# Kernel optimization log

Hardware: AMD Instinct MI355X
Metric: run time of the kernel (lower is better)

Reference implementation:

```python
import jax, jax.numpy as jnp
import numpy as np

# dims
B, V, IMG = 16, 2, 224
G, PATCH, SG = 7, 14, 16
D, NH, L = 768, 12, 12
DH = D // NH            # 64
P = DH // 4             # rope frequencies per axis (2D axial RoPE)
N = G * G               # 49 glimpse tokens
S = SG * SG             # 256 scene tokens
GSIZE = G * PATCH       # 98 px glimpse


def _ln(x, w, b):
    m = x.mean(-1, keepdims=True)
    v = ((x - m) ** 2).mean(-1, keepdims=True)
    return (x - m) * jax.lax.rsqrt(v + 1e-6) * w + b


def _rope(pos, periods):
    # pos [B,N,2] -> cos,sin [B,N,2P]  (x freqs then y freqs)
    ang = (pos[..., :, None] / periods).reshape(pos.shape[0], pos.shape[1], -1)
    return jnp.cos(ang), jnp.sin(ang)


def _apply_rope(x, cos, sin):
    # x [B,H,N,DH]; cos/sin [B,N,DH//2]
    c = cos[:, None, :, :]
    s = sin[:, None, :, :]
    xr = x.reshape(x.shape[0], x.shape[1], x.shape[2], DH // 2, 2)
    x1, x2 = xr[..., 0], xr[..., 1]
    return jnp.stack([x1 * c - x2 * s, x1 * s + x2 * c], -1).reshape(x.shape)


def _heads(x):
    return x.reshape(x.shape[0], x.shape[1], NH, DH).transpose(0, 2, 1, 3)


def _merge(x):
    return x.transpose(0, 2, 1, 3).reshape(x.shape[0], x.shape[2], D)


def _attn(q, k, v):
    a = jax.nn.softmax(jnp.einsum('bhqd,bhkd->bhqk', q, k) / jnp.sqrt(jnp.float32(DH)), axis=-1)
    return jnp.einsum('bhqk,bhkd->bhqd', a, v)


def _cross(xq, xkv, qw, qb, kvw, kvb, ow, ob, rq, rkv):
    q = _heads(xq @ qw.T + qb)
    kv = xkv @ kvw.T + kvb
    k, v = _heads(kv[..., :D]), _heads(kv[..., D:])
    q = _apply_rope(q, *rq)
    k = _apply_rope(k, *rkv)
    return _merge(_attn(q, k, v)) @ ow.T + ob


def _bilinear(img, py, px):
    # img [C,H,W], py/px [GSIZE] pixel coords -> [C,GSIZE,GSIZE]
    Hh, Ww = img.shape[1], img.shape[2]
    y0 = jnp.clip(jnp.floor(py), 0, Hh - 2).astype(jnp.int32)
    x0 = jnp.clip(jnp.floor(px), 0, Ww - 2).astype(jnp.int32)
    wy = jnp.clip(py - y0, 0.0, 1.0)[None, :, None]
    wx = jnp.clip(px - x0, 0.0, 1.0)[None, None, :]
    g0, g1 = img[:, y0, :], img[:, y0 + 1, :]
    v00, v01 = g0[:, :, x0], g0[:, :, x0 + 1]
    v10, v11 = g1[:, :, x0], g1[:, :, x0 + 1]
    return (v00 * (1 - wy) + v10 * wy) * (1 - wx) + (v01 * (1 - wy) + v11 * wy) * wx


def _extract(images, c, s):
    # crop a [-1,1]-normalized glimpse of half-width `scale` at `center`
    lin = jnp.linspace(-1.0, 1.0, GSIZE)
    gy = c[:, 1:2] + s[:, None] * lin
    gx = c[:, 0:1] + s[:, None] * lin
    py = (gy + 1.0) * 0.5 * (images.shape[2] - 1)
    px = (gx + 1.0) * 0.5 * (images.shape[3] - 1)
    return jax.vmap(_bilinear)(images, py, px)


def _forward(images, centers, scales, patch_w, patch_b, scene_tokens,
             ln1_w, ln1_b, ln2_w, ln2_b, qkv_w, qkv_b, attn_out_w, attn_out_b,
             mlp_w1, mlp_b1, mlp_w2, mlp_b2,
             read_q_w, read_q_b, read_kv_w, read_kv_b, read_out_w, read_out_b, read_gate,
             write_q_w, write_q_b, write_kv_w, write_kv_b, write_out_w, write_out_b, write_gate):
    periods = 100.0 ** (jnp.arange(P, dtype=jnp.float32) / P)
    lin_s = jnp.linspace(-1.0, 1.0, SG)
    ys, xs = jnp.meshgrid(lin_s, lin_s, indexing='ij')
    scene_pos = jnp.broadcast_to(jnp.stack([xs.ravel(), ys.ravel()], -1), (B, S, 2))
    scene_rope = _rope(scene_pos, periods)
    lin_g = jnp.linspace(-1.0, 1.0, G)
    yg, xg = jnp.meshgrid(lin_g, lin_g, indexing='ij')
    goffs = jnp.stack([xg.ravel(), yg.ravel()], -1)  # [N,2]

    scene = jnp.broadcast_to(scene_tokens, (B, S, D))
    for vp in range(V):
        glimpse = _extract(images, centers[vp], scales[vp])  # [B,3,98,98]
        t = jax.lax.conv_general_dilated(glimpse, patch_w, (PATCH, PATCH), 'VALID',
                                         dimension_numbers=('NCHW', 'OIHW', 'NCHW'))
        local = t.reshape(B, D, N).transpose(0, 2, 1) + patch_b  # [B,49,D]
        lpos = centers[vp][:, None, :] + scales[vp][:, None, None] * goffs
        lrope = _rope(lpos, periods)
        for i in range(L):
            local = local + read_gate[i] * _cross(local, scene,
                read_q_w[i], read_q_b[i], read_kv_w[i], read_kv_b[i],
                read_out_w[i], read_out_b[i], lrope, scene_rope)
            # ViT block with RoPE self-attention
            h = _ln(local, ln1_w[i], ln1_b[i])
            qkv = h @ qkv_w[i].T + qkv_b[i]
            q, k, v = _heads(qkv[..., :D]), _heads(qkv[..., D:2 * D]), _heads(qkv[..., 2 * D:])
            q = _apply_rope(q, *lrope)
            k = _apply_rope(k, *lrope)
            local = local + _merge(_attn(q, k, v)) @ attn_out_w[i].T + attn_out_b[i]
            h = _ln(local, ln2_w[i], ln2_b[i])
            local = local + jax.nn.gelu(h @ mlp_w1[i].T + mlp_b1[i]) @ mlp_w2[i].T + mlp_b2[i]
            scene = scene + write_gate[i] * _cross(scene, local,
                write_q_w[i], write_q_b[i], write_kv_w[i], write_kv_b[i],
                write_out_w[i], write_out_b[i], scene_rope, lrope)
    return scene  # [B,S,D]


def setup_inputs() -> dict:
    key = jax.random.key(0)
    ks = iter(jax.random.split(key, 40))
    std = 0.02
    d = {}
    d['images'] = jax.random.normal(next(ks), (B, 3, IMG, IMG), jnp.float32)
    d['centers'] = jax.random.uniform(next(ks), (V, B, 2), jnp.float32, -0.5, 0.5)
    d['scales'] = jax.random.uniform(next(ks), (V, B), jnp.float32, 0.2, 0.4)
    d['patch_w'] = jax.random.normal(next(ks), (D, 3, PATCH, PATCH), jnp.float32) * std
    d['patch_b'] = jnp.zeros((D,), jnp.float32)
    d['scene_tokens'] = jax.random.normal(next(ks), (1, S, D), jnp.float32) / jnp.sqrt(jnp.float32(D))
    d['ln1_w'] = jnp.ones((L, D), jnp.float32); d['ln1_b'] = jnp.zeros((L, D), jnp.float32)
    d['ln2_w'] = jnp.ones((L, D), jnp.float32); d['ln2_b'] = jnp.zeros((L, D), jnp.float32)
    d['qkv_w'] = jax.random.normal(next(ks), (L, 3 * D, D), jnp.float32) * std
    d['qkv_b'] = jnp.zeros((L, 3 * D), jnp.float32)
    d['attn_out_w'] = jax.random.normal(next(ks), (L, D, D), jnp.float32) * std
    d['attn_out_b'] = jnp.zeros((L, D), jnp.float32)
    d['mlp_w1'] = jax.random.normal(next(ks), (L, 4 * D, D), jnp.float32) * std
    d['mlp_b1'] = jnp.zeros((L, 4 * D), jnp.float32)
    d['mlp_w2'] = jax.random.normal(next(ks), (L, D, 4 * D), jnp.float32) * std
    d['mlp_b2'] = jnp.zeros((L, D), jnp.float32)
    for pre in ('read', 'write'):
        d[pre + '_q_w'] = jax.random.normal(next(ks), (L, D, D), jnp.float32) * std
        d[pre + '_q_b'] = jnp.zeros((L, D), jnp.float32)
        d[pre + '_kv_w'] = jax.random.normal(next(ks), (L, 2 * D, D), jnp.float32) * std
        d[pre + '_kv_b'] = jnp.zeros((L, 2 * D), jnp.float32)
        d[pre + '_out_w'] = jax.random.normal(next(ks), (L, D, D), jnp.float32) * std
        d[pre + '_out_b'] = jnp.zeros((L, D), jnp.float32)
        d[pre + '_gate'] = jax.random.normal(next(ks), (L, D), jnp.float32) * 0.1
    return d


def reference(images, centers, scales, patch_w, patch_b, scene_tokens,
              ln1_w, ln1_b, ln2_w, ln2_b, qkv_w, qkv_b, attn_out_w, attn_out_b,
              mlp_w1, mlp_b1, mlp_w2, mlp_b2,
              read_q_w, read_q_b, read_kv_w, read_kv_b, read_out_w, read_out_b, read_gate,
              write_q_w, write_q_b, write_kv_w, write_kv_b, write_out_w, write_out_b, write_gate):
    return _forward(images, centers, scales, patch_w, patch_b, scene_tokens,
                    ln1_w, ln1_b, ln2_w, ln2_b, qkv_w, qkv_b, attn_out_w, attn_out_b,
                    mlp_w1, mlp_b1, mlp_w2, mlp_b2,
                    read_q_w, read_q_b, read_kv_w, read_kv_b, read_out_w, read_out_b, read_gate,
                    write_q_w, write_q_b, write_kv_w, write_kv_b, write_out_w, write_out_b, write_gate)
```

## Files before the change

kernel.cpp:

```cpp
#include <hip/hip_runtime.h>

#define B_ 16
#define V_ 2
#define D_ 768
#define NH_ 12
#define L_ 12
#define DH_ 64
#define N_ 49
#define S_ 256

__device__ __forceinline__ unsigned short f2bf(float f) {
  unsigned int u = __builtin_bit_cast(unsigned int, f);
  u += 0x7fffu + ((u >> 16) & 1u);
  return (unsigned short)(u >> 16);
}
__device__ __forceinline__ float bf2f(unsigned short h) {
  unsigned int u = ((unsigned int)h) << 16;
  return __builtin_bit_cast(float, u);
}
__device__ __forceinline__ float bflo(unsigned int w) {
  return __builtin_bit_cast(float, w << 16);
}
__device__ __forceinline__ float bfhi(unsigned int w) {
  return __builtin_bit_cast(float, w & 0xffff0000u);
}
__device__ __forceinline__ unsigned int packbf2(float a, float b) {
  return (unsigned int)f2bf(a) | ((unsigned int)f2bf(b) << 16);
}

using bf16x8 = __attribute__((ext_vector_type(8))) __bf16;
using u16x8  = __attribute__((ext_vector_type(8))) unsigned short;
using f32x4  = __attribute__((ext_vector_type(4))) float;

__device__ __forceinline__ void g2l16(const unsigned short* g, unsigned short* l) {
  __builtin_amdgcn_global_load_lds(
      (const __attribute__((address_space(1))) unsigned int*)g,
      (__attribute__((address_space(3))) unsigned int*)l, 16, 0, 0);
}

template <int BM, int BN, int BK>
__global__ __launch_bounds__(256) void gemm_v4(
    const unsigned short* __restrict__ A, int lda,
    const unsigned short* __restrict__ W, int ldw,
    const float* __restrict__ bias,
    float* __restrict__ Cf, unsigned short* __restrict__ Cb, int ldc,
    const float* __restrict__ res, const float* __restrict__ gate,
    int M, int N, int K, int epi)
{
  __shared__ unsigned short As[2][BM * BK];
  __shared__ unsigned short Bs[2][BN * BK];
  constexpr int FM = BM / 32, FN = BN / 32;
  constexpr int CPR = BK / 8;
  constexpr int LPS = (BM + BN) * BK / 2048;
  const int m0 = blockIdx.x * BM, n0 = blockIdx.y * BN;
  const int tid = threadIdx.x, lane = tid & 63, wid = tid >> 6;
  const int wr = wid >> 1, wc = wid & 1;
  const int fr = lane & 15, kq8 = lane >> 4;

  f32x4 acc[FM][FN];
#pragma unroll
  for (int mi = 0; mi < FM; ++mi)
#pragma unroll
    for (int ni = 0; ni < FN; ++ni) acc[mi][ni] = f32x4{0.f, 0.f, 0.f, 0.f};

  auto stage = [&](int buf, int k0) {
    const unsigned short* Ab = A + (size_t)m0 * lda + k0;
    const unsigned short* Bb = W + (size_t)n0 * ldw + k0;
#pragma unroll
    for (int ra = 0; ra < BM * BK / 2048; ++ra) {
      int c = ra * 256 + tid;
      int row = c / CPR, slot = c % CPR;
      int gslot = slot ^ (row & 7);
      g2l16(Ab + (size_t)row * lda + gslot * 8, &As[buf][c * 8]);
    }
#pragma unroll
    for (int rb = 0; rb < BN * BK / 2048; ++rb) {
      int c = rb * 256 + tid;
      int row = c / CPR, slot = c % CPR;
      int gslot = slot ^ (row & 7);
      g2l16(Bb + (size_t)row * ldw + gslot * 8, &Bs[buf][c * 8]);
    }
  };

  const int nt = K / BK;
  stage(0, 0);
  int cur = 0;
  for (int t = 0; t < nt; ++t) {
    if (t + 1 < nt) {
      stage(cur ^ 1, (t + 1) * BK);
      asm volatile("s_waitcnt vmcnt(%0)" :: "i"(LPS) : "memory");
    } else {
      asm volatile("s_waitcnt vmcnt(0)" ::: "memory");
    }
    __builtin_amdgcn_s_barrier();
#pragma unroll
    for (int ks = 0; ks < BK / 32; ++ks) {
      bf16x8 av[FM], bv[FN];
#pragma unroll
      for (int mi = 0; mi < FM; ++mi) {
        int row = wr * (BM / 2) + mi * 16 + fr;
        int idx = row * BK + (((ks * 4 + kq8) ^ (row & 7)) << 3);
        av[mi] = __builtin_bit_cast(bf16x8, *(const u16x8*)&As[cur][idx]);
      }
#pragma unroll
      for (int ni = 0; ni < FN; ++ni) {
        int row = wc * (BN / 2) + ni * 16 + fr;
        int idx = row * BK + (((ks * 4 + kq8) ^ (row & 7)) << 3);
        bv[ni] = __builtin_bit_cast(bf16x8, *(const u16x8*)&Bs[cur][idx]);
      }
#pragma unroll
      for (int mi = 0; mi < FM; ++mi)
#pragma unroll
        for (int ni = 0; ni < FN; ++ni)
          acc[mi][ni] = __builtin_amdgcn_mfma_f32_16x16x32_bf16(av[mi], bv[ni], acc[mi][ni], 0, 0, 0);
    }
    __builtin_amdgcn_s_barrier();
    cur ^= 1;
  }

  const int er = (lane >> 4) * 4, ec = lane & 15;
#pragma unroll
  for (int mi = 0; mi < FM; ++mi)
#pragma unroll
    for (int ni = 0; ni < FN; ++ni) {
      int gc = n0 + wc * (BN / 2) + ni * 16 + ec;
      float bi = bias ? bias[gc] : 0.0f;
      float gg = gate ? gate[gc] : 1.0f;
#pragma unroll
      for (int i = 0; i < 4; ++i) {
        int gr = m0 + wr * (BM / 2) + mi * 16 + er + i;
        if (gr < M) {
          float v = acc[mi][ni][i] + bi;
          if (epi == 1) {
            v = v / (1.0f + __expf(-1.59576912f * (v + 0.044715f * v * v * v)));
          } else if (epi == 2) {
            v = res[(size_t)gr * ldc + gc] + gg * v;
          }
          if (Cf) Cf[(size_t)gr * ldc + gc] = v;
          if (Cb) Cb[(size_t)gr * ldc + gc] = f2bf(v);
        }
      }
    }
}

template <int LKPAD>
__global__ __launch_bounds__(256) void attn_mfma(
    const unsigned short* __restrict__ Q, int ldq, int qoff, int Lq,
    const unsigned short* __restrict__ KV, int ldkv, int koff, int voff, int Lk,
    const float* __restrict__ cq, const float* __restrict__ sq, int rbq,
    const float* __restrict__ ck, const float* __restrict__ sk, int rbk,
    unsigned short* __restrict__ Out)
{
  constexpr int NT = LKPAD / 16;
  constexpr int NKS = LKPAD / 32;
  __shared__ unsigned short Kb[LKPAD * 64];
  __shared__ unsigned short Vt[64 * LKPAD];
  __shared__ unsigned short Qs[4][16 * 64];
  __shared__ unsigned short Pl[4][16 * LKPAD];
  const int b = blockIdx.x / NH_, h = blockIdx.x - b * NH_;
  const int tid = threadIdx.x, lane = tid & 63, wid = tid >> 6;

  for (int idx = tid; idx < LKPAD * 32; idx += 256) {
    int t = idx >> 5, m = idx & 31;
    int d = 2 * m;
    int ksl = (t << 6) + (((m >> 2) ^ (t & 7)) << 3) + ((m & 3) << 1);
    int vs0 = d * LKPAD + (((t >> 3) ^ (d & 7)) << 3) + (t & 7);
    int vs1 = (d + 1) * LKPAD + (((t >> 3) ^ ((d + 1) & 7)) << 3) + (t & 7);
    if (t < Lk) {
      size_t rowb = ((size_t)b * Lk + t) * ldkv;
      unsigned int kw = *(const unsigned int*)(KV + rowb + koff + h * DH_ + d);
      unsigned int vw = *(const unsigned int*)(KV + rowb + voff + h * DH_ + d);
      float k1 = bflo(kw), k2 = bfhi(kw);
      size_t ri = (size_t)b * rbk + (size_t)t * 32 + m;
      float c = ck[ri], s = sk[ri];
      *(unsigned int*)&Kb[ksl] = packbf2((k1 * c - k2 * s) * 0.125f, (k1 * s + k2 * c) * 0.125f);
      Vt[vs0] = (unsigned short)(vw & 0xffff);
      Vt[vs1] = (unsigned short)(vw >> 16);
    } else {
      *(unsigned int*)&Kb[ksl] = 0;
      Vt[vs0] = 0; Vt[vs1] = 0;
    }
  }
  const int qbase = blockIdx.y * 64 + wid * 16;
  for (int idx = lane; idx < 16 * 32; idx += 64) {
    int r = idx >> 5, m = idx & 31;
    int gq = qbase + r;
    unsigned int qr = 0;
    if (gq < Lq) {
      unsigned int qw = *(const unsigned int*)(Q + ((size_t)b * Lq + gq) * ldq + qoff + h * DH_ + 2 * m);
      float q1 = bflo(qw), q2 = bfhi(qw);
      size_t ri = (size_t)b * rbq + (size_t)gq * 32 + m;
      float c = cq[ri], s = sq[ri];
      qr = packbf2(q1 * c - q2 * s, q1 * s + q2 * c);
    }
    *(unsigned int*)&Qs[wid][(r << 6) + (((m >> 2) ^ (r & 7)) << 3) + ((m & 3) << 1)] = qr;
  }
  __syncthreads();

  const int fr = lane & 15, g = lane >> 4;
  bf16x8 qa[2];
#pragma unroll
  for (int ks = 0; ks < 2; ++ks)
    qa[ks] = __builtin_bit_cast(bf16x8,
        *(const u16x8*)&Qs[wid][(fr << 6) + ((((ks << 2) + g) ^ (fr & 7)) << 3)]);

  f32x4 sv[NT];
  __builtin_amdgcn_s_setprio(1);
#pragma unroll
  for (int t = 0; t < NT; ++t) {
    int key = (t << 4) + fr;
    f32x4 a = {0.f, 0.f, 0.f, 0.f};
#pragma unroll
    for (int ks = 0; ks < 2; ++ks) {
      bf16x8 kb = __builtin_bit_cast(bf16x8,
          *(const u16x8*)&Kb[(key << 6) + ((((ks << 2) + g) ^ (key & 7)) << 3)]);
      a = __builtin_amdgcn_mfma_f32_16x16x32_bf16(qa[ks], kb, a, 0, 0, 0);
    }
    sv[t] = a;
  }
  __builtin_amdgcn_s_setprio(0);
#pragma unroll
  for (int t = 0; t < NT; ++t) {
    int key = (t << 4) + fr;
    if (key >= Lk) sv[t] = f32x4{-1e30f, -1e30f, -1e30f, -1e30f};
  }
  f32x4 mx = sv[0];
#pragma unroll
  for (int t = 1; t < NT; ++t)
#pragma unroll
    for (int i = 0; i < 4; ++i) mx[i] = fmaxf(mx[i], sv[t][i]);
#pragma unroll
  for (int off = 1; off <= 8; off <<= 1)
#pragma unroll
    for (int i = 0; i < 4; ++i) mx[i] = fmaxf(mx[i], __shfl_xor(mx[i], off));
  f32x4 sm = {0.f, 0.f, 0.f, 0.f};
#pragma unroll
  for (int t = 0; t < NT; ++t)
#pragma unroll
    for (int i = 0; i < 4; ++i) {
      float e = __expf(sv[t][i] - mx[i]);
      sv[t][i] = e;
      sm[i] += e;
    }
#pragma unroll
  for (int off = 1; off <= 8; off <<= 1)
#pragma unroll
    for (int i = 0; i < 4; ++i) sm[i] += __shfl_xor(sm[i], off);
  f32x4 inv;
#pragma unroll
  for (int i = 0; i < 4; ++i) inv[i] = 1.0f / sm[i];
#pragma unroll
  for (int t = 0; t < NT; ++t) {
    int key = (t << 4) + fr;
    int chunk = key >> 3;
#pragma unroll
    for (int i = 0; i < 4; ++i) {
      int row = (g << 2) + i;
      Pl[wid][row * LKPAD + ((chunk ^ (row & 7)) << 3) + (key & 7)] = f2bf(sv[t][i]);
    }
  }
  f32x4 oacc[4];
#pragma unroll
  for (int n = 0; n < 4; ++n) oacc[n] = f32x4{0.f, 0.f, 0.f, 0.f};
  __builtin_amdgcn_s_setprio(1);
#pragma unroll
  for (int ks = 0; ks < NKS; ++ks) {
    int chunk = (ks << 2) + g;
    bf16x8 pa = __builtin_bit_cast(bf16x8,
        *(const u16x8*)&Pl[wid][fr * LKPAD + ((chunk ^ (fr & 7)) << 3)]);
#pragma unroll
    for (int n = 0; n < 4; ++n) {
      int drow = (n << 4) + fr;
      bf16x8 vb = __builtin_bit_cast(bf16x8,
          *(const u16x8*)&Vt[drow * LKPAD + ((chunk ^ (drow & 7)) << 3)]);
      oacc[n] = __builtin_amdgcn_mfma_f32_16x16x32_bf16(pa, vb, oacc[n], 0, 0, 0);
    }
  }
  __builtin_amdgcn_s_setprio(0);
#pragma unroll
  for (int n = 0; n < 4; ++n)
#pragma unroll
    for (int i = 0; i < 4; ++i) {
      int gq = qbase + (g << 2) + i;
      if (gq < Lq)
        Out[((size_t)b * Lq + gq) * D_ + h * DH_ + (n << 4) + fr] = f2bf(oacc[n][i] * inv[i]);
    }
}

__global__ __launch_bounds__(256) void ln_kernel(
    const float* __restrict__ X, const float* __restrict__ w,
    const float* __restrict__ bsh, unsigned short* __restrict__ Out)
{
  const int row = blockIdx.x, tid = threadIdx.x;
  const float* x = X + (size_t)row * D_;
  float v0 = x[tid], v1 = x[tid + 256], v2 = x[tid + 512];
  __shared__ float red[4];
  float s = v0 + v1 + v2;
  for (int o = 32; o; o >>= 1) s += __shfl_xor(s, o);
  if ((tid & 63) == 0) red[tid >> 6] = s;
  __syncthreads();
  float mean = (red[0] + red[1] + red[2] + red[3]) * (1.0f / 768.0f);
  float d0 = v0 - mean, d1 = v1 - mean, d2 = v2 - mean;
  float q = d0 * d0 + d1 * d1 + d2 * d2;
  __syncthreads();
  for (int o = 32; o; o >>= 1) q += __shfl_xor(q, o);
  if ((tid & 63) == 0) red[tid >> 6] = q;
  __syncthreads();
  float var = (red[0] + red[1] + red[2] + red[3]) * (1.0f / 768.0f);
  float rstd = rsqrtf(var + 1e-6f);
  Out[(size_t)row * D_ + tid]       = f2bf(d0 * rstd * w[tid]       + bsh[tid]);
  Out[(size_t)row * D_ + tid + 256] = f2bf(d1 * rstd * w[tid + 256] + bsh[tid + 256]);
  Out[(size_t)row * D_ + tid + 512] = f2bf(d2 * rstd * w[tid + 512] + bsh[tid + 512]);
}

struct CvtA {
  const float* s[10];
  unsigned short* d[10];
  unsigned int lsrc[10];
  unsigned int lstride[10];
  int blkEnd[10];
};
__global__ __launch_bounds__(256) void cvt_multi_k(CvtA c) {
  int bid = blockIdx.x;
  int seg = 0;
#pragma unroll
  for (int i = 0; i < 9; ++i) seg += (bid >= c.blkEnd[i]) ? 1 : 0;
  unsigned int e = (unsigned int)(bid - (seg ? c.blkEnd[seg - 1] : 0)) * 2048u
                   + (unsigned int)threadIdx.x * 8u;
  unsigned int l = e / c.lsrc[seg], r = e - l * c.lsrc[seg];
  const float* s = c.s[seg] + e;
  unsigned short* d = c.d[seg] + (size_t)l * c.lstride[seg] + r;
  f32x4 a = *(const f32x4*)s, b2 = *(const f32x4*)(s + 4);
  u16x8 o;
  o[0] = f2bf(a.x); o[1] = f2bf(a.y); o[2] = f2bf(a.z); o[3] = f2bf(a.w);
  o[4] = f2bf(b2.x); o[5] = f2bf(b2.y); o[6] = f2bf(b2.z); o[7] = f2bf(b2.w);
  *(u16x8*)d = o;
}

__global__ void cvt_patch_k(const float* __restrict__ s, unsigned short* __restrict__ d) {
  int i = blockIdx.x * 256 + threadIdx.x;
  if (i >= 768 * 768) return;
  int r = i / 768, col = i - r * 768;
  d[i] = f2bf(col < 588 ? s[r * 588 + col] : 0.0f);
}

__global__ void fbias_k(const float* __restrict__ wqb, const float* __restrict__ rkvb,
                        float* __restrict__ fb) {
  int i = blockIdx.x * 256 + threadIdx.x;
  if (i >= L_ * 2304) return;
  int l = i / 2304, c = i - l * 2304;
  fb[i] = (c < 768) ? wqb[l * 768 + c] : rkvb[l * 1536 + (c - 768)];
}

__global__ void init_scene_k(const float* __restrict__ tok, float* __restrict__ sf,
                             unsigned short* __restrict__ sb, int total) {
  int i = blockIdx.x * 256 + threadIdx.x;
  if (i < total) {
    float v = tok[i % (S_ * D_)];
    sf[i] = v; sb[i] = f2bf(v);
  }
}

__global__ void rope_scene_k(float* __restrict__ c, float* __restrict__ s) {
  int idx = blockIdx.x * 256 + threadIdx.x;
  if (idx >= S_ * 32) return;
  int t = idx >> 5, m = idx & 31;
  int i = t >> 4, j = t & 15;
  float xx = -1.0f + 2.0f * j / 15.0f;
  float yy = -1.0f + 2.0f * i / 15.0f;
  float coord = (m < 16) ? xx : yy;
  float per = powf(100.0f, (float)(m & 15) / 16.0f);
  float ang = coord / per;
  c[idx] = cosf(ang); s[idx] = sinf(ang);
}

__global__ void rope_local_k(float* __restrict__ c, float* __restrict__ s,
                             const float* __restrict__ ctr, const float* __restrict__ scl) {
  int idx = blockIdx.x * 256 + threadIdx.x;
  if (idx >= B_ * N_ * 32) return;
  int b = idx / (N_ * 32);
  int r = idx - b * (N_ * 32);
  int pch = r >> 5, m = r & 31;
  int py = pch / 7, px = pch - py * 7;
  float cx = ctr[b * 2], cy = ctr[b * 2 + 1], sc = scl[b];
  float gx = cx + sc * ((px - 3.0f) / 3.0f);
  float gy = cy + sc * ((py - 3.0f) / 3.0f);
  float coord = (m < 16) ? gx : gy;
  float per = powf(100.0f, (float)(m & 15) / 16.0f);
  float ang = coord / per;
  c[idx] = cosf(ang); s[idx] = sinf(ang);
}

__global__ void im2col_k(unsigned short* __restrict__ xb, const float* __restrict__ img,
                         const float* __restrict__ ctr, const float* __restrict__ scl) {
  int idx = blockIdx.x * 256 + threadIdx.x;
  if (idx >= 784 * 768) return;
  int row = idx / 768, col = idx - row * 768;
  float val = 0.0f;
  if (col < 588) {
    int b = row / 49, pch = row - b * 49;
    int c = col / 196, rr = col - c * 196;
    int i = rr / 14, j = rr - i * 14;
    int py = pch / 7, px = pch - py * 7;
    int gyi = py * 14 + i, gxi = px * 14 + j;
    float cx = ctr[b * 2], cy = ctr[b * 2 + 1], sc = scl[b];
    float gy = cy + sc * (-1.0f + 2.0f * gyi / 97.0f);
    float gx = cx + sc * (-1.0f + 2.0f * gxi / 97.0f);
    float pyi = (gy + 1.0f) * 0.5f * 223.0f;
    float pxi = (gx + 1.0f) * 0.5f * 223.0f;
    float y0f = fminf(fmaxf(floorf(pyi), 0.0f), 222.0f);
    float x0f = fminf(fmaxf(floorf(pxi), 0.0f), 222.0f);
    int y0 = (int)y0f, x0 = (int)x0f;
    float wy = fminf(fmaxf(pyi - y0f, 0.0f), 1.0f);
    float wx = fminf(fmaxf(pxi - x0f, 0.0f), 1.0f);
    const float* base = img + (size_t)(b * 3 + c) * 224 * 224;
    float v00 = base[y0 * 224 + x0],       v01 = base[y0 * 224 + x0 + 1];
    float v10 = base[(y0 + 1) * 224 + x0], v11 = base[(y0 + 1) * 224 + x0 + 1];
    val = (v00 * (1.0f - wy) + v10 * wy) * (1.0f - wx) + (v01 * (1.0f - wy) + v11 * wy) * wx;
  }
  xb[idx] = f2bf(val);
}

extern "C" void kernel_launch(void* const* d_in, const int* in_sizes, int n_in,
                              void* d_out, int out_size, void* d_ws, size_t ws_size,
                              hipStream_t stream) {
  const float* images    = (const float*)d_in[0];
  const float* centers   = (const float*)d_in[1];
  const float* scales    = (const float*)d_in[2];
  const float* patch_w   = (const float*)d_in[3];
  const float* patch_b   = (const float*)d_in[4];
  const float* scene_tok = (const float*)d_in[5];
  const float* ln1_w = (const float*)d_in[6];
  const float* ln1_b = (const float*)d_in[7];
  const float* ln2_w = (const float*)d_in[8];
  const float* ln2_b = (const float*)d_in[9];
  const float* qkv_w = (const float*)d_in[10];
  const float* qkv_b = (const float*)d_in[11];
  const float* ao_w  = (const float*)d_in[12];
  const float* ao_b  = (const float*)d_in[13];
  const float* m1_w  = (const float*)d_in[14];
  const float* m1_b  = (const float*)d_in[15];
  const float* m2_w  = (const float*)d_in[16];
  const float* m2_b  = (const float*)d_in[17];
  const float* rq_w  = (const float*)d_in[18];
  const float* rq_b  = (const float*)d_in[19];
  const float* rkv_w = (const float*)d_in[20];
  const float* rkv_b = (const float*)d_in[21];
  const float* ro_w  = (const float*)d_in[22];
  const float* ro_b  = (const float*)d_in[23];
  const float* rgate = (const float*)d_in[24];
  const float* wq_w  = (const float*)d_in[25];
  const float* wq_b  = (const float*)d_in[26];
  const float* wkv_w = (const float*)d_in[27];
  const float* wkv_b = (const float*)d_in[28];
  const float* wo_w  = (const float*)d_in[29];
  const float* wo_b  = (const float*)d_in[30];
  const float* wgate = (const float*)d_in[31];

  float* scene_f = (float*)d_out;

  char* p = (char*)d_ws;
  auto alloc = [&](size_t bytes) { char* r = p; p += (bytes + 255) & ~(size_t)255; return (void*)r; };
  unsigned short* scene_bf = (unsigned short*)alloc((size_t)4096 * 768 * 2);
  float*          local_f  = (float*)alloc((size_t)784 * 768 * 4);
  unsigned short* local_bf = (unsigned short*)alloc((size_t)832 * 768 * 2);
  unsigned short* q_r_bf   = (unsigned short*)alloc((size_t)784 * 768 * 2);
  unsigned short* qrkv_bf  = (unsigned short*)alloc((size_t)4096 * 2304 * 2);
  unsigned short* kv_bf    = (unsigned short*)alloc((size_t)784 * 2304 * 2);
  unsigned short* ln_bf    = (unsigned short*)alloc((size_t)832 * 768 * 2);
  unsigned short* act_bf   = (unsigned short*)alloc((size_t)4096 * 768 * 2);
  unsigned short* x_bf     = (unsigned short*)alloc((size_t)832 * 768 * 2);
  float* sc_cos = (float*)alloc((size_t)S_ * 32 * 4);
  float* sc_sin = (float*)alloc((size_t)S_ * 32 * 4);
  float* l_cos  = (float*)alloc((size_t)B_ * N_ * 32 * 4);
  float* l_sin  = (float*)alloc((size_t)B_ * N_ * 32 * 4);
  unsigned short* patch_wbf = (unsigned short*)alloc((size_t)768 * 768 * 2);
  float*          fb        = (float*)alloc((size_t)L_ * 2304 * 4);

  static const unsigned int LSRC[10] = {589824, 589824, 1179648, 589824, 1769472,
                                        589824, 2359296, 2359296, 1179648, 589824};
  static const unsigned int LSTR[10] = {589824, 1769472, 1769472, 589824, 1769472,
                                        589824, 2359296, 2359296, 1179648, 589824};
  static const unsigned int DOFF[10] = {0, 0, 589824, 0, 0, 0, 0, 0, 0, 0};
  const float* WSRC[10] = {rq_w, wq_w, rkv_w, ro_w, qkv_w, ao_w, m1_w, m2_w, wkv_w, wo_w};
  static const size_t REGSZ[9] = {589824, 1769472, 589824, 1769472, 589824,
                                  2359296, 2359296, 1179648, 589824};
  size_t regBase[9];
  size_t allElemsPerLayer = 0;
  {
    size_t cur = 0;
    for (int i = 0; i < 9; ++i) { regBase[i] = cur; cur += REGSZ[i] * L_; allElemsPerLayer += REGSZ[i]; }
  }
  const size_t allElems = allElemsPerLayer * L_;
  size_t usedBytes = (size_t)(p - (char*)d_ws);
  bool preconv = ws_size >= usedBytes + allElems * 2 + 4096;
  unsigned short* wbf = (unsigned short*)alloc((preconv ? allElems : allElemsPerLayer) * 2);

  enum { T128, T128x64, T64 };
  auto G = [&](int tile, const unsigned short* A, int lda, const unsigned short* Wp, int ldw,
               const float* bias, float* Cf, unsigned short* Cb, int ldc,
               const float* res, const float* gt, int M, int N, int K, int epi) {
    if (tile == T128)
      gemm_v4<128, 128, 64><<<dim3(M / 128, N / 128), 256, 0, stream>>>(
          A, lda, Wp, ldw, bias, Cf, Cb, ldc, res, gt, M, N, K, epi);
    else if (tile == T128x64)
      gemm_v4<128, 64, 64><<<dim3(M / 128, N / 64), 256, 0, stream>>>(
          A, lda, Wp, ldw, bias, Cf, Cb, ldc, res, gt, M, N, K, epi);
    else
      gemm_v4<64, 64, 128><<<dim3((M + 63) / 64, N / 64), 256, 0, stream>>>(
          A, lda, Wp, ldw, bias, Cf, Cb, ldc, res, gt, M, N, K, epi);
  };

  {
    int total = B_ * S_ * D_;
    init_scene_k<<<(total + 255) / 256, 256, 0, stream>>>(scene_tok, scene_f, scene_bf, total);
    rope_scene_k<<<(S_ * 32 + 255) / 256, 256, 0, stream>>>(sc_cos, sc_sin);
    cvt_patch_k<<<(768 * 768 + 255) / 256, 256, 0, stream>>>(patch_w, patch_wbf);
    fbias_k<<<(L_ * 2304 + 255) / 256, 256, 0, stream>>>(wq_b, rkv_b, fb);
    if (preconv) {
      CvtA cv;
      int blk = 0;
      for (int i = 0; i < 10; ++i) {
        int reg = i >= 2 ? i - 1 : i;
        cv.s[i] = WSRC[i];
        cv.d[i] = wbf + regBase[reg] + DOFF[i];
        cv.lsrc[i] = LSRC[i];
        cv.lstride[i] = LSTR[i];
        blk += (int)((size_t)LSRC[i] * L_ / 2048);
        cv.blkEnd[i] = blk;
      }
      cvt_multi_k<<<blk, 256, 0, stream>>>(cv);
    }
  }

  for (int vp = 0; vp < V_; ++vp) {
    const float* ctr = centers + (size_t)vp * B_ * 2;
    const float* scl = scales + (size_t)vp * B_;
    rope_local_k<<<(B_ * N_ * 32 + 255) / 256, 256, 0, stream>>>(l_cos, l_sin, ctr, scl);
    im2col_k<<<(784 * 768 + 255) / 256, 256, 0, stream>>>(x_bf, images, ctr, scl);
    G(T64, x_bf, 768, patch_wbf, 768, patch_b, local_f, local_bf, 768,
      nullptr, nullptr, 784, 768, 768, 0);

    for (int l = 0; l < L_; ++l) {
      const unsigned short* wL[10];
      if (preconv) {
        for (int i = 0; i < 10; ++i) {
          int reg = i >= 2 ? i - 1 : i;
          wL[i] = wbf + regBase[reg] + (size_t)l * LSTR[i] + DOFF[i];
        }
      } else {
        CvtA cv;
        int blk = 0;
        size_t cur = 0;
        size_t rb[9];
        for (int i = 0; i < 10; ++i) {
          int reg = i >= 2 ? i - 1 : i;
          if (i != 2) { rb[reg] = cur; cur += REGSZ[reg]; }
          cv.s[i] = WSRC[i] + (size_t)l * LSRC[i];
          cv.d[i] = wbf + rb[reg] + DOFF[i];
          cv.lsrc[i] = LSRC[i];
          cv.lstride[i] = LSTR[i];
          blk += (int)(LSRC[i] / 2048);
          cv.blkEnd[i] = blk;
          wL[i] = (unsigned short*)cv.d[i];
        }
        cvt_multi_k<<<blk, 256, 0, stream>>>(cv);
      }
      const unsigned short *w_rq = wL[0], *w_qrkv = wL[1], *w_ro = wL[3], *w_qkv = wL[4],
                           *w_ao = wL[5], *w_m1 = wL[6], *w_m2 = wL[7], *w_wkv = wL[8],
                           *w_wo = wL[9];

      G(T128, scene_bf, 768, w_qrkv, 768, fb + (size_t)l * 2304,
        nullptr, qrkv_bf, 2304, nullptr, nullptr, 4096, 2304, 768, 0);
      G(T64, local_bf, 768, w_rq, 768, rq_b + l * 768,
        nullptr, q_r_bf, 768, nullptr, nullptr, 784, 768, 768, 0);
      attn_mfma<256><<<dim3(B_ * NH_, 1), 256, 0, stream>>>(q_r_bf, 768, 0, 49,
          qrkv_bf, 2304, 768, 1536, 256, l_cos, l_sin, N_ * 32, sc_cos, sc_sin, 0, act_bf);
      G(T64, act_bf, 768, w_ro, 768, ro_b + l * 768,
        local_f, local_bf, 768, local_f, rgate + l * 768, 784, 768, 768, 2);
      ln_kernel<<<784, 256, 0, stream>>>(local_f, ln1_w + l * 768, ln1_b + l * 768, ln_bf);
      G(T64, ln_bf, 768, w_qkv, 768, qkv_b + (size_t)l * 2304,
        nullptr, kv_bf, 2304, nullptr, nullptr, 784, 2304, 768, 0);
      attn_mfma<64><<<dim3(B_ * NH_, 1), 256, 0, stream>>>(kv_bf, 2304, 0, 49,
          kv_bf, 2304, 768, 1536, 49, l_cos, l_sin, N_ * 32, l_cos, l_sin, N_ * 32, act_bf);
      G(T64, act_bf, 768, w_ao, 768, ao_b + l * 768,
        local_f, local_bf, 768, local_f, nullptr, 784, 768, 768, 2);
      ln_kernel<<<784, 256, 0, stream>>>(local_f, ln2_w + l * 768, ln2_b + l * 768, ln_bf);
      G(T64, ln_bf, 768, w_m1, 768, m1_b + (size_t)l * 3072,
        nullptr, act_bf, 3072, nullptr, nullptr, 784, 3072, 768, 1);
      G(T64, act_bf, 3072, w_m2, 3072, m2_b + l * 768,
        local_f, local_bf, 768, local_f, nullptr, 784, 768, 3072, 2);
      G(T64, local_bf, 768, w_wkv, 768, wkv_b + (size_t)l * 1536,
        nullptr, kv_bf, 1536, nullptr, nullptr, 784, 1536, 768, 0);
      attn_mfma<64><<<dim3(B_ * NH_, 4), 256, 0, stream>>>(qrkv_bf, 2304, 0, 256,
          kv_bf, 1536, 0, 768, 49, sc_cos, sc_sin, 0, l_cos, l_sin, N_ * 32, act_bf);
      G(T128x64, act_bf, 768, w_wo, 768, wo_b + l * 768,
        scene_f, scene_bf, 768, scene_f, wgate + l * 768, 4096, 768, 768, 2);
    }
  }
}
```

Before: 6.534 ms.

## Fuse next-layer read-Q into write-KV GEMM, swizzle GEMM workgroups across XCDs, retile

Adds an XCD-aware remapping of workgroup ids in the GEMM so neighbouring tiles land on the same chiplet, aiming for better L2 reuse. The next layer's read-query projection weights are concatenated onto the write-KV weights, so one GEMM yields both and the separate read-Q GEMM runs only at layer 0. GEMM tiles change to BK=128 with 128x128 for scene GEMMs and 128x64 for local ones. Local buffers are padded to 896 rows for the larger M tile. This adds bias and weight layout complexity and may reduce occupancy through the larger LDS tiles.

```diff
diff --git a/kernel.cpp b/kernel.cpp
--- a/kernel.cpp
+++ b/kernel.cpp
@@ -39,7 +39,7 @@
 }
 
 template <int BM, int BN, int BK>
-__global__ __launch_bounds__(256) void gemm_v4(
+__global__ __launch_bounds__(256) void gemm_v5(
     const unsigned short* __restrict__ A, int lda,
     const unsigned short* __restrict__ W, int ldw,
     const float* __restrict__ bias,
@@ -52,7 +52,14 @@
   constexpr int FM = BM / 32, FN = BN / 32;
   constexpr int CPR = BK / 8;
   constexpr int LPS = (BM + BN) * BK / 2048;
-  const int m0 = blockIdx.x * BM, n0 = blockIdx.y * BN;
+  const int gx = gridDim.x;
+  const int nwg = gx * gridDim.y;
+  const int orig = blockIdx.y * gx + blockIdx.x;
+  const int xcd = orig & 7, rem = orig >> 3;
+  const int qq = nwg >> 3, rr = nwg & 7;
+  const int wgid = (xcd < rr ? xcd * (qq + 1) : rr * (qq + 1) + (xcd - rr) * qq) + rem;
+  const int m0 = (wgid % gx) * BM, n0 = (wgid / gx) * BN;
+
   const int tid = threadIdx.x, lane = tid & 63, wid = tid >> 6;
   const int wr = wid >> 1, wc = wid & 1;
   const int fr = lane & 15, kq8 = lane >> 4;
@@ -314,17 +321,17 @@
 }
 
 struct CvtA {
-  const float* s[10];
-  unsigned short* d[10];
-  unsigned int lsrc[10];
-  unsigned int lstride[10];
-  int blkEnd[10];
+  const float* s[11];
+  unsigned short* d[11];
+  unsigned int lsrc[11];
+  unsigned int lstride[11];
+  int blkEnd[11];
 };
 __global__ __launch_bounds__(256) void cvt_multi_k(CvtA c) {
   int bid = blockIdx.x;
   int seg = 0;
 #pragma unroll
-  for (int i = 0; i < 9; ++i) seg += (bid >= c.blkEnd[i]) ? 1 : 0;
+  for (int i = 0; i < 10; ++i) seg += (bid >= c.blkEnd[i]) ? 1 : 0;
   unsigned int e = (unsigned int)(bid - (seg ? c.blkEnd[seg - 1] : 0)) * 2048u
                    + (unsigned int)threadIdx.x * 8u;
   unsigned int l = e / c.lsrc[seg], r = e - l * c.lsrc[seg];
@@ -350,6 +357,14 @@
   if (i >= L_ * 2304) return;
   int l = i / 2304, c = i - l * 2304;
   fb[i] = (c < 768) ? wqb[l * 768 + c] : rkvb[l * 1536 + (c - 768)];
+}
+
+__global__ void fbias2_k(const float* __restrict__ wkvb, const float* __restrict__ rqb,
+                         float* __restrict__ fb2) {
+  int i = blockIdx.x * 256 + threadIdx.x;
+  if (i >= L_ * 2304) return;
+  int l = i / 2304, c = i - l * 2304;
+  fb2[i] = (c < 1536) ? wkvb[l * 1536 + c] : rqb[((l + 1) % L_) * 768 + (c - 1536)];
 }
 
 __global__ void init_scene_k(const float* __restrict__ tok, float* __restrict__ sf,
@@ -463,52 +478,60 @@
   auto alloc = [&](size_t bytes) { char* r = p; p += (bytes + 255) & ~(size_t)255; return (void*)r; };
   unsigned short* scene_bf = (unsigned short*)alloc((size_t)4096 * 768 * 2);
   float*          local_f  = (float*)alloc((size_t)784 * 768 * 4);
-  unsigned short* local_bf = (unsigned short*)alloc((size_t)832 * 768 * 2);
-  unsigned short* q_r_bf   = (unsigned short*)alloc((size_t)784 * 768 * 2);
+  unsigned short* local_bf = (unsigned short*)alloc((size_t)896 * 768 * 2);
+  unsigned short* q_r_bf   = (unsigned short*)alloc((size_t)896 * 768 * 2);
   unsigned short* qrkv_bf  = (unsigned short*)alloc((size_t)4096 * 2304 * 2);
-  unsigned short* kv_bf    = (unsigned short*)alloc((size_t)784 * 2304 * 2);
-  unsigned short* ln_bf    = (unsigned short*)alloc((size_t)832 * 768 * 2);
+  unsigned short* kv_bf    = (unsigned short*)alloc((size_t)896 * 2304 * 2);
+  unsigned short* kvq_bf   = (unsigned short*)alloc((size_t)896 * 2304 * 2);
+  unsigned short* ln_bf    = (unsigned short*)alloc((size_t)896 * 768 * 2);
   unsigned short* act_bf   = (unsigned short*)alloc((size_t)4096 * 768 * 2);
-  unsigned short* x_bf     = (unsigned short*)alloc((size_t)832 * 768 * 2);
+  unsigned short* x_bf     = (unsigned short*)alloc((size_t)896 * 768 * 2);
   float* sc_cos = (float*)alloc((size_t)S_ * 32 * 4);
   float* sc_sin = (float*)alloc((size_t)S_ * 32 * 4);
   float* l_cos  = (float*)alloc((size_t)B_ * N_ * 32 * 4);
   float* l_sin  = (float*)alloc((size_t)B_ * N_ * 32 * 4);
   unsigned short* patch_wbf = (unsigned short*)alloc((size_t)768 * 768 * 2);
   float*          fb        = (float*)alloc((size_t)L_ * 2304 * 4);
-
-  static const unsigned int LSRC[10] = {589824, 589824, 1179648, 589824, 1769472,
-                                        589824, 2359296, 2359296, 1179648, 589824};
-  static const unsigned int LSTR[10] = {589824, 1769472, 1769472, 589824, 1769472,
-                                        589824, 2359296, 2359296, 1179648, 589824};
-  static const unsigned int DOFF[10] = {0, 0, 589824, 0, 0, 0, 0, 0, 0, 0};
-  const float* WSRC[10] = {rq_w, wq_w, rkv_w, ro_w, qkv_w, ao_w, m1_w, m2_w, wkv_w, wo_w};
+  float*          fb2       = (float*)alloc((size_t)L_ * 2304 * 4);
+
   static const size_t REGSZ[9] = {589824, 1769472, 589824, 1769472, 589824,
-                                  2359296, 2359296, 1179648, 589824};
+                                  2359296, 2359296, 1769472, 589824};
+  struct SegDef { const float* src; int reg; unsigned off; unsigned lsrc; int nl; };
+  const SegDef SEGS[11] = {
+    {rq_w,            0, 0,       589824,  L_},
+    {wq_w,            1, 0,       589824,  L_},
+    {rkv_w,           1, 589824,  1179648, L_},
+    {ro_w,            2, 0,       589824,  L_},
+    {qkv_w,           3, 0,       1769472, L_},
+    {ao_w,            4, 0,       589824,  L_},
+    {m1_w,            5, 0,       2359296, L_},
+    {m2_w,            6, 0,       2359296, L_},
+    {wkv_w,           7, 0,       1179648, L_},
+    {rq_w + 589824,   7, 1179648, 589824,  L_ - 1},
+    {wo_w,            8, 0,       589824,  L_},
+  };
   size_t regBase[9];
-  size_t allElemsPerLayer = 0;
+  size_t perLayer = 0;
   {
     size_t cur = 0;
-    for (int i = 0; i < 9; ++i) { regBase[i] = cur; cur += REGSZ[i] * L_; allElemsPerLayer += REGSZ[i]; }
-  }
-  const size_t allElems = allElemsPerLayer * L_;
+    for (int i = 0; i < 9; ++i) { regBase[i] = cur; cur += REGSZ[i] * L_; perLayer += REGSZ[i]; }
+  }
+  const size_t allElems = perLayer * L_;
   size_t usedBytes = (size_t)(p - (char*)d_ws);
   bool preconv = ws_size >= usedBytes + allElems * 2 + 4096;
-  unsigned short* wbf = (unsigned short*)alloc((preconv ? allElems : allElemsPerLayer) * 2);
-
-  enum { T128, T128x64, T64 };
-  auto G = [&](int tile, const unsigned short* A, int lda, const unsigned short* Wp, int ldw,
-               const float* bias, float* Cf, unsigned short* Cb, int ldc,
-               const float* res, const float* gt, int M, int N, int K, int epi) {
-    if (tile == T128)
-      gemm_v4<128, 128, 64><<<dim3(M / 128, N / 128), 256, 0, stream>>>(
-          A, lda, Wp, ldw, bias, Cf, Cb, ldc, res, gt, M, N, K, epi);
-    else if (tile == T128x64)
-      gemm_v4<128, 64, 64><<<dim3(M / 128, N / 64), 256, 0, stream>>>(
-          A, lda, Wp, ldw, bias, Cf, Cb, ldc, res, gt, M, N, K, epi);
-    else
-      gemm_v4<64, 64, 128><<<dim3((M + 63) / 64, N / 64), 256, 0, stream>>>(
-          A, lda, Wp, ldw, bias, Cf, Cb, ldc, res, gt, M, N, K, epi);
+  unsigned short* wbf = (unsigned short*)alloc((preconv ? allElems : perLayer) * 2);
+
+  auto GQ = [&](const unsigned short* A, int lda, const unsigned short* Wp,
+                const float* bias, float* Cf, unsigned short* Cb, int ldc,
+                const float* res, const float* gt, int M, int N, int epi) {
+    gemm_v5<128, 128, 128><<<dim3(M / 128, N / 128), 256, 0, stream>>>(
+        A, lda, Wp, 768, bias, Cf, Cb, ldc, res, gt, M, N, 768, epi);
+  };
+  auto GS = [&](const unsigned short* A, int lda, const unsigned short* Wp, int ldw,
+                const float* bias, float* Cf, unsigned short* Cb, int ldc,
+                const float* res, const float* gt, int N, int K, int epi) {
+    gemm_v5<128, 64, 128><<<dim3(7, N / 64), 256, 0, stream>>>(
+        A, lda, Wp, ldw, bias, Cf, Cb, ldc, res, gt, 784, N, K, epi);
   };
 
   {
@@ -517,16 +540,16 @@
     rope_scene_k<<<(S_ * 32 + 255) / 256, 256, 0, stream>>>(sc_cos, sc_sin);
     cvt_patch_k<<<(768 * 768 + 255) / 256, 256, 0, stream>>>(patch_w, patch_wbf);
     fbias_k<<<(L_ * 2304 + 255) / 256, 256, 0, stream>>>(wq_b, rkv_b, fb);
+    fbias2_k<<<(L_ * 2304 + 255) / 256, 256, 0, stream>>>(wkv_b, rq_b, fb2);
     if (preconv) {
       CvtA cv;
       int blk = 0;
-      for (int i = 0; i < 10; ++i) {
-        int reg = i >= 2 ? i - 1 : i;
-        cv.s[i] = WSRC[i];
-        cv.d[i] = wbf + regBase[reg] + DOFF[i];
-        cv.lsrc[i] = LSRC[i];
-        cv.lstride[i] = LSTR[i];
-        blk += (int)((size_t)LSRC[i] * L_ / 2048);
+      for (int i = 0; i < 11; ++i) {
+        cv.s[i] = SEGS[i].src;
+        cv.d[i] = wbf + regBase[SEGS[i].reg] + SEGS[i].off;
+        cv.lsrc[i] = SEGS[i].lsrc;
+        cv.lstride[i] = (unsigned)REGSZ[SEGS[i].reg];
+        blk += (int)((size_t)SEGS[i].lsrc * SEGS[i].nl / 2048);
         cv.blkEnd[i] = blk;
       }
       cvt_multi_k<<<blk, 256, 0, stream>>>(cv);
@@ -538,64 +561,63 @@
     const float* scl = scales + (size_t)vp * B_;
     rope_local_k<<<(B_ * N_ * 32 + 255) / 256, 256, 0, stream>>>(l_cos, l_sin, ctr, scl);
     im2col_k<<<(784 * 768 + 255) / 256, 256, 0, stream>>>(x_bf, images, ctr, scl);
-    G(T64, x_bf, 768, patch_wbf, 768, patch_b, local_f, local_bf, 768,
-      nullptr, nullptr, 784, 768, 768, 0);
+    GS(x_bf, 768, patch_wbf, 768, patch_b, local_f, local_bf, 768,
+       nullptr, nullptr, 768, 768, 0);
 
     for (int l = 0; l < L_; ++l) {
-      const unsigned short* wL[10];
+      const unsigned short* wR[9];
       if (preconv) {
-        for (int i = 0; i < 10; ++i) {
-          int reg = i >= 2 ? i - 1 : i;
-          wL[i] = wbf + regBase[reg] + (size_t)l * LSTR[i] + DOFF[i];
-        }
+        for (int rg = 0; rg < 9; ++rg)
+          wR[rg] = wbf + regBase[rg] + (size_t)l * REGSZ[rg];
       } else {
         CvtA cv;
         int blk = 0;
         size_t cur = 0;
         size_t rb[9];
-        for (int i = 0; i < 10; ++i) {
-          int reg = i >= 2 ? i - 1 : i;
-          if (i != 2) { rb[reg] = cur; cur += REGSZ[reg]; }
-          cv.s[i] = WSRC[i] + (size_t)l * LSRC[i];
-          cv.d[i] = wbf + rb[reg] + DOFF[i];
-          cv.lsrc[i] = LSRC[i];
-          cv.lstride[i] = LSTR[i];
-          blk += (int)(LSRC[i] / 2048);
+        for (int rg = 0; rg < 9; ++rg) { rb[rg] = cur; cur += REGSZ[rg]; wR[rg] = wbf + rb[rg]; }
+        for (int i = 0; i < 11; ++i) {
+          size_t srcl = (i == 9) ? (size_t)((l + 1) % L_) : (size_t)l;
+          cv.s[i] = (i == 9 ? rq_w : SEGS[i].src) + srcl * SEGS[i].lsrc;
+          cv.d[i] = wbf + rb[SEGS[i].reg] + SEGS[i].off;
+          cv.lsrc[i] = SEGS[i].lsrc;
+          cv.lstride[i] = (unsigned)REGSZ[SEGS[i].reg];
+          blk += (int)(SEGS[i].lsrc / 2048);
           cv.blkEnd[i] = blk;
-          wL[i] = (unsigned short*)cv.d[i];
         }
         cvt_multi_k<<<blk, 256, 0, stream>>>(cv);
       }
-      const unsigned short *w_rq = wL[0], *w_qrkv = wL[1], *w_ro = wL[3], *w_qkv = wL[4],
-                           *w_ao = wL[5], *w_m1 = wL[6], *w_m2 = wL[7], *w_wkv = wL[8],
-                           *w_wo = wL[9];
-
-      G(T128, scene_bf, 768, w_qrkv, 768, fb + (size_t)l * 2304,
-        nullptr, qrkv_bf, 2304, nullptr, nullptr, 4096, 2304, 768, 0);
-      G(T64, local_bf, 768, w_rq, 768, rq_b + l * 768,
-        nullptr, q_r_bf, 768, nullptr, nullptr, 784, 768, 768, 0);
-      attn_mfma<256><<<dim3(B_ * NH_, 1), 256, 0, stream>>>(q_r_bf, 768, 0, 49,
-          qrkv_bf, 2304, 768, 1536, 256, l_cos, l_sin, N_ * 32, sc_cos, sc_sin, 0, act_bf);
-      G(T64, act_bf, 768, w_ro, 768, ro_b + l * 768,
-        local_f, local_bf, 768, local_f, rgate + l * 768, 784, 768, 768, 2);
+
+      GQ(scene_bf, 768, wR[1], fb + (size_t)l * 2304,
+         nullptr, qrkv_bf, 2304, nullptr, nullptr, 4096, 2304, 0);
+      if (l == 0)
+        GS(local_bf, 768, wR[0], 768, rq_b + l * 768,
+           nullptr, q_r_bf, 768, nullptr, nullptr, 768, 768, 0);
+      if (l == 0)
+        attn_mfma<256><<<dim3(B_ * NH_, 1), 256, 0, stream>>>(q_r_bf, 768, 0, 49,
+            qrkv_bf, 2304, 768, 1536, 256, l_cos, l_sin, N_ * 32, sc_cos, sc_sin, 0, act_bf);
+      else
+        attn_mfma<256><<<dim3(B_ * NH_, 1), 256, 0, stream>>>(kvq_bf, 2304, 1536, 49,
+            qrkv_bf, 2304, 768, 1536, 256, l_cos, l_sin, N_ * 32, sc_cos, sc_sin, 0, act_bf);
+      GS(act_bf, 768, wR[2], 768, ro_b + l * 768,
+         local_f, local_bf, 768, local_f, rgate + l * 768, 768, 768, 2);
       ln_kernel<<<784, 256, 0, stream>>>(local_f, ln1_w + l * 768, ln1_b + l * 768, ln_bf);
-      G(T64, ln_bf, 768, w_qkv, 768, qkv_b + (size_t)l * 2304,
-        nullptr, kv_bf, 2304, nullptr, nullptr, 784, 2304, 768, 0);
+      GS(ln_bf, 768, wR[3], 768, qkv_b + (size_t)l * 2304,
+         nullptr, kv_bf, 2304, nullptr, nullptr, 2304, 768, 0);
       attn_mfma<64><<<dim3(B_ * NH_, 1), 256, 0, stream>>>(kv_bf, 2304, 0, 49,
           kv_bf, 2304, 768, 1536, 49, l_cos, l_sin, N_ * 32, l_cos, l_sin, N_ * 32, act_bf);
-      G(T64, act_bf, 768, w_ao, 768, ao_b + l * 768,
-        local_f, local_bf, 768, local_f, nullptr, 784, 768, 768, 2);
+      GS(act_bf, 768, wR[4], 768, ao_b + l * 768,
+         local_f, local_bf, 768, local_f, nullptr, 768, 768, 2);
       ln_kernel<<<784, 256, 0, stream>>>(local_f, ln2_w + l * 768, ln2_b + l * 768, ln_bf);
-      G(T64, ln_bf, 768, w_m1, 768, m1_b + (size_t)l * 3072,
-        nullptr, act_bf, 3072, nullptr, nullptr, 784, 3072, 768, 1);
-      G(T64, act_bf, 3072, w_m2, 3072, m2_b + l * 768,
-        local_f, local_bf, 768, local_f, nullptr, 784, 768, 3072, 2);
-      G(T64, local_bf, 768, w_wkv, 768, wkv_b + (size_t)l * 1536,
-        nullptr, kv_bf, 1536, nullptr, nullptr, 784, 1536, 768, 0);
+      GS(ln_bf, 768, wR[5], 768, m1_b + (size_t)l * 3072,
+         nullptr, act_bf, 3072, nullptr, nullptr, 3072, 768, 1);
+      GS(act_bf, 3072, wR[6], 3072, m2_b + l * 768,
+         local_f, local_bf, 768, local_f, nullptr, 768, 3072, 2);
+      GS(local_bf, 768, wR[7], 768, fb2 + (size_t)l * 2304,
+         nullptr, kvq_bf, 2304, nullptr, nullptr, 2304, 768, 0);
       attn_mfma<64><<<dim3(B_ * NH_, 4), 256, 0, stream>>>(qrkv_bf, 2304, 0, 256,
-          kv_bf, 1536, 0, 768, 49, sc_cos, sc_sin, 0, l_cos, l_sin, N_ * 32, act_bf);
-      G(T128x64, act_bf, 768, w_wo, 768, wo_b + l * 768,
-        scene_f, scene_bf, 768, scene_f, wgate + l * 768, 4096, 768, 768, 2);
-    }
-  }
-}
+          kvq_bf, 2304, 0, 768, 49, sc_cos, sc_sin, 0, l_cos, l_sin, N_ * 32, act_bf);
+      GQ(act_bf, 768, wR[8], wo_b + l * 768,
+         scene_f, scene_bf, 768, scene_f, wgate + l * 768, 4096, 768, 2);
+    }
+  }
+}
```

Measured after the change: 8.232 ms. +26.0%, slower.
